# Kernel optimization log

Hardware: AMD Instinct MI355X
Metric: run time of the kernel (lower is better)

## Reference

```python
import jax, jax.numpy as jnp
import numpy as np

TAU_CONVERGE = 0.01
N_STABLE = 2
B, L, DIM = 8, 4096, 1024
H, M = 16, 64
D_HEAD = DIM // H


def setup_inputs() -> dict:
    key = jax.random.key(0)
    k1, k2, k3, k4, k5, k6 = jax.random.split(key, 6)
    z_current = jax.random.normal(k1, (B, L, DIM), dtype=jnp.float32)
    # small perturbation so per-head velocity straddles tau_converge
    z_prev = z_current + 0.00125 * jax.random.normal(k2, (B, L, DIM), dtype=jnp.float32)
    codebook = jax.random.normal(k3, (H, M, D_HEAD), dtype=jnp.float32) * 0.02
    frozen_values = jax.random.normal(k4, (B, L, H, D_HEAD), dtype=jnp.float32)
    consecutive_converged = jax.random.randint(k5, (B, L, H), 0, 2, dtype=jnp.int32)
    crystallised = jax.random.randint(k6, (B, L, H), 0, 2) > 0
    return {
        "z_current": z_current,
        "z_prev": z_prev,
        "codebook": codebook,
        "frozen_values": frozen_values,
        "consecutive_converged": consecutive_converged,
        "crystallised": crystallised,
    }


def reference(z_current, z_prev, codebook, frozen_values, consecutive_converged, crystallised):
    """One crystallisation step: velocity -> counters -> snap-to-codebook -> enforce.

    Mirrors ConvergenceMonitor.update_and_crystallise followed by enforce(),
    with MultiHeadedCodebook.quantise(hard=True) for the codebook snap.
    All freeze/snap logic is outside the gradient graph (torch.no_grad/detach).
    """
    sg = jax.lax.stop_gradient
    zc = z_current.reshape(B, L, H, D_HEAD)   # [B,L,H,d]
    zp = z_prev.reshape(B, L, H, D_HEAD)

    # per-head velocity norm (detached in original)
    velocity = jnp.linalg.norm(sg(zc) - sg(zp), axis=-1)       # [B,L,H]
    converged = velocity < TAU_CONVERGE
    cc_new = jnp.where(converged, consecutive_converged + 1, 0)
    newly = (cc_new >= N_STABLE) & (~crystallised)             # [B,L,H] bool

    # hard nearest-neighbour quantise per head (no_grad in original)
    z_sg = sg(zc)
    cb = sg(codebook)
    # squared L2 distance: ||z||^2 - 2 z.c + ||c||^2  -> [B,L,H,M]
    d2 = (jnp.sum(z_sg * z_sg, axis=-1, keepdims=True)
          - 2.0 * jnp.einsum('blhd,hmd->blhm', z_sg, cb)
          + jnp.sum(cb * cb, axis=-1)[None, None])
    idx = jnp.argmin(d2, axis=-1)                              # [B,L,H]
    # gather nearest entries per head: codebook[h, idx[b,l,h]] -> [B,L,H,d]
    entries = cb[jnp.arange(H)[None, None, :], idx]

    # masked scatter of newly crystallised heads into frozen values
    frozen_new = jnp.where(newly[..., None], entries, sg(frozen_values))
    crystal_new = crystallised | newly

    # enforce: overwrite crystallised heads with frozen codebook values
    z_enforced = jnp.where(crystal_new[..., None], frozen_new, zc).reshape(B, L, DIM)
    return z_enforced, crystal_new, newly, cc_new, frozen_new
```

## Files before the change

### kernel.cpp

```cpp
#include <hip/hip_runtime.h>

#define BB 8
#define LL 4096
#define DIM 1024
#define HH 16
#define MM 64
#define DH 64

constexpr long long NZ = (long long)BB * LL * DIM;
constexpr long long NG = (long long)BB * LL * HH;
constexpr long long O_Z   = 0;
constexpr long long O_CRY = NZ;
constexpr long long O_NEW = NZ + NG;
constexpr long long O_CC  = NZ + 2 * NG;
constexpr long long O_FR  = NZ + 3 * NG;

#define DETECT_BLOCKS 64
#define DETECT_DWORDS (NG / 4)

__global__ __launch_bounds__(256) void detect_bool_kernel(
    const unsigned int* __restrict__ buf, unsigned int* __restrict__ partials)
{
    __shared__ unsigned int acc;
    if (threadIdx.x == 0) acc = 0u;
    __syncthreads();
    const int per_block = DETECT_DWORDS / DETECT_BLOCKS;
    const long long base = (long long)blockIdx.x * per_block;
    unsigned int v = 0u;
    for (int i = threadIdx.x; i < per_block; i += 256)
        v |= buf[base + i];
    atomicOr(&acc, v);
    __syncthreads();
    if (threadIdx.x == 0) partials[blockIdx.x] = acc;
}

#define ROWS 8

__global__ __launch_bounds__(256) void crystal_main(
    const float4* __restrict__ zc4,
    const float4* __restrict__ zp4,
    const float4* __restrict__ fr4,
    const int*    __restrict__ ccount,
    const void*   __restrict__ cry_raw,
    const unsigned int* __restrict__ partials,
    float* __restrict__ out)
{
    const int t   = threadIdx.x;
    const int h   = t >> 4;
    const int sub = t & 15;

    unsigned int om = 0u;
    #pragma unroll
    for (int i = 0; i < DETECT_BLOCKS; ++i) om |= partials[i];
    const bool u8mode = om > 1u;

    const long long row0 = (long long)blockIdx.x * ROWS;
    long long idx = row0 * (DIM / 4) + t;
    long long g   = row0 * HH + h;

    float4 zc = zc4[idx];
    float4 zp = zp4[idx];
    float4 fr = fr4[idx];
    int    cc = ccount[g];
    int    cv = u8mode ? (int)((const unsigned char*)cry_raw)[g]
                       : ((const int*)cry_raw)[g];

    #pragma unroll 1
    for (int r = 0; r < ROWS; ++r) {
        const long long nidx = idx + (DIM / 4);
        const long long gn   = g + HH;
        float4 zcn, zpn, frn; int ccn_ = 0, cvn = 0;
        if (r < ROWS - 1) {
            zcn = zc4[nidx]; zpn = zp4[nidx]; frn = fr4[nidx];
            ccn_ = ccount[gn];
            cvn  = u8mode ? (int)((const unsigned char*)cry_raw)[gn]
                          : ((const int*)cry_raw)[gn];
        }

        double s;
        {
            double dx = (double)zc.x - (double)zp.x;
            double dy = (double)zc.y - (double)zp.y;
            double dz = (double)zc.z - (double)zp.z;
            double dw = (double)zc.w - (double)zp.w;
            s = dx * dx + dy * dy + dz * dz + dw * dw;
        }
        s += __shfl_xor(s, 1);
        s += __shfl_xor(s, 2);
        s += __shfl_xor(s, 4);
        s += __shfl_xor(s, 8);

        const bool conv = sqrt(s) < 0.01;
        const int  ccn  = conv ? cc + 1 : 0;
        const bool cry  = cv != 0;
        const bool newly   = (ccn >= 2) && !cry;
        const bool crystal = cry || newly;

        float4 zout;
        zout.x = crystal ? fr.x : zc.x;
        zout.y = crystal ? fr.y : zc.y;
        zout.z = crystal ? fr.z : zc.z;
        zout.w = crystal ? fr.w : zc.w;

        reinterpret_cast<float4*>(out + O_Z)[idx]  = zout;
        reinterpret_cast<float4*>(out + O_FR)[idx] = fr;
        if (sub == 0) {
            out[O_CRY + g] = crystal ? 1.0f : 0.0f;
            out[O_NEW + g] = newly   ? 1.0f : 0.0f;
            out[O_CC  + g] = (float)ccn;
        }

        zc = zcn; zp = zpn; fr = frn; cc = ccn_; cv = cvn;
        idx = nidx; g = gn;
    }
}

#define RPB 64
#define CHUNKS (BB * LL / RPB)

__global__ __launch_bounds__(64) void crystal_snap(
    const float4* __restrict__ zc4,
    const float*  __restrict__ cb,
    float* __restrict__ out)
{
    __shared__ float zsh[DH];

    const int lane = threadIdx.x;
    const int h    = blockIdx.x / CHUNKS;
    const int c    = blockIdx.x % CHUNKS;
    const long long blbase = (long long)c * RPB;

    const float f = out[O_NEW + (blbase + lane) * HH + h];
    unsigned long long mask = __ballot(f > 0.5f);
    if (mask == 0ull) return;

    const float* cbh = cb + (long long)h * MM * DH;
    const float4* crow = reinterpret_cast<const float4*>(cbh + lane * DH);

    while (mask) {
        const int r = __ffsll(mask) - 1;
        mask &= mask - 1;
        const long long bl   = blbase + r;
        const long long seg4 = bl * (DIM / 4) + h * (DH / 4);

        if (lane < 16)
            reinterpret_cast<float4*>(zsh)[lane] = zc4[seg4 + lane];
        __syncthreads();

        double d2 = 0.0;
        #pragma unroll
        for (int k = 0; k < DH / 4; ++k) {
            const float4 zk = reinterpret_cast<const float4*>(zsh)[k];
            const float4 cvv = crow[k];
            double a = (double)zk.x - (double)cvv.x;
            double b = (double)zk.y - (double)cvv.y;
            double cq = (double)zk.z - (double)cvv.z;
            double d = (double)zk.w - (double)cvv.w;
            d2 += a * a + b * b + cq * cq + d * d;
        }

        double best = d2;
        int bidx = lane;
        #pragma unroll
        for (int m2 = 1; m2 <= 32; m2 <<= 1) {
            double ob = __shfl_xor(best, m2);
            int    oi = __shfl_xor(bidx, m2);
            if (ob < best || (ob == best && oi < bidx)) { best = ob; bidx = oi; }
        }

        if (lane < 16) {
            const float4 ev = reinterpret_cast<const float4*>(cbh + bidx * DH)[lane];
            reinterpret_cast<float4*>(out + O_Z)[seg4 + lane]  = ev;
            reinterpret_cast<float4*>(out + O_FR)[seg4 + lane] = ev;
        }
        __syncthreads();
    }
}

extern "C" void kernel_launch(void* const* d_in, const int* in_sizes, int n_in,
                              void* d_out, int out_size, void* d_ws, size_t ws_size,
                              hipStream_t stream) {
    const float4* zc4 = (const float4*)d_in[0];
    const float4* zp4 = (const float4*)d_in[1];
    const float*  cb  = (const float*)d_in[2];
    const float4* fr4 = (const float4*)d_in[3];
    const int*    cc  = (const int*)d_in[4];
    const void*   cry = d_in[5];
    float* out = (float*)d_out;
    unsigned int* partials = (unsigned int*)d_ws;

    hipLaunchKernelGGL(detect_bool_kernel, dim3(DETECT_BLOCKS), dim3(256), 0, stream,
                       (const unsigned int*)cry, partials);
    hipLaunchKernelGGL(crystal_main, dim3((BB * LL) / ROWS), dim3(256), 0, stream,
                       zc4, zp4, fr4, cc, cry, partials, out);
    hipLaunchKernelGGL(crystal_snap, dim3(HH * CHUNKS), dim3(64), 0, stream,
                       zc4, cb, out);
}
```

Baseline: 218.6 us.

## Drop bool-detect pass, emit newly bitmasks, streamline snap kernel

```diff
diff --git a/kernel.cpp b/kernel.cpp
--- a/kernel.cpp
+++ b/kernel.cpp
@@ -15,24 +15,8 @@
 constexpr long long O_CC  = NZ + 2 * NG;
 constexpr long long O_FR  = NZ + 3 * NG;
 
-#define DETECT_BLOCKS 64
-#define DETECT_DWORDS (NG / 4)
-
-__global__ __launch_bounds__(256) void detect_bool_kernel(
-    const unsigned int* __restrict__ buf, unsigned int* __restrict__ partials)
-{
-    __shared__ unsigned int acc;
-    if (threadIdx.x == 0) acc = 0u;
-    __syncthreads();
-    const int per_block = DETECT_DWORDS / DETECT_BLOCKS;
-    const long long base = (long long)blockIdx.x * per_block;
-    unsigned int v = 0u;
-    for (int i = threadIdx.x; i < per_block; i += 256)
-        v |= buf[base + i];
-    atomicOr(&acc, v);
-    __syncthreads();
-    if (threadIdx.x == 0) partials[blockIdx.x] = acc;
-}
+typedef float nfloat4 __attribute__((ext_vector_type(4)));
+
 
 #define ROWS 8
 
@@ -41,18 +25,17 @@
     const float4* __restrict__ zp4,
     const float4* __restrict__ fr4,
     const int*    __restrict__ ccount,
-    const void*   __restrict__ cry_raw,
-    const unsigned int* __restrict__ partials,
+    const int*    __restrict__ cryst,
+    unsigned int* __restrict__ masks,
     float* __restrict__ out)
 {
+    __shared__ float lds_cry[ROWS * HH];
+    __shared__ float lds_new[ROWS * HH];
+    __shared__ float lds_cc [ROWS * HH];
+
     const int t   = threadIdx.x;
     const int h   = t >> 4;
     const int sub = t & 15;
-
-    unsigned int om = 0u;
-    #pragma unroll
-    for (int i = 0; i < DETECT_BLOCKS; ++i) om |= partials[i];
-    const bool u8mode = om > 1u;
 
     const long long row0 = (long long)blockIdx.x * ROWS;
     long long idx = row0 * (DIM / 4) + t;
@@ -62,8 +45,9 @@
     float4 zp = zp4[idx];
     float4 fr = fr4[idx];
     int    cc = ccount[g];
-    int    cv = u8mode ? (int)((const unsigned char*)cry_raw)[g]
-                       : ((const int*)cry_raw)[g];
+    int    cv = cryst[g];
+
+    unsigned int wmask = 0u;
 
     #pragma unroll 1
     for (int r = 0; r < ROWS; ++r) {
@@ -72,9 +56,7 @@
         float4 zcn, zpn, frn; int ccn_ = 0, cvn = 0;
         if (r < ROWS - 1) {
             zcn = zc4[nidx]; zpn = zp4[nidx]; frn = fr4[nidx];
-            ccn_ = ccount[gn];
-            cvn  = u8mode ? (int)((const unsigned char*)cry_raw)[gn]
-                          : ((const int*)cry_raw)[gn];
+            ccn_ = ccount[gn]; cvn = cryst[gn];
         }
 
         double s;
@@ -96,66 +78,113 @@
         const bool newly   = (ccn >= 2) && !cry;
         const bool crystal = cry || newly;
 
-        float4 zout;
+        nfloat4 zout;
         zout.x = crystal ? fr.x : zc.x;
         zout.y = crystal ? fr.y : zc.y;
         zout.z = crystal ? fr.z : zc.z;
         zout.w = crystal ? fr.w : zc.w;
-
-        reinterpret_cast<float4*>(out + O_Z)[idx]  = zout;
-        reinterpret_cast<float4*>(out + O_FR)[idx] = fr;
+        nfloat4 frv = { fr.x, fr.y, fr.z, fr.w };
+
+        __builtin_nontemporal_store(zout, reinterpret_cast<nfloat4*>(out + O_Z)  + idx);
+        __builtin_nontemporal_store(frv,  reinterpret_cast<nfloat4*>(out + O_FR) + idx);
+
         if (sub == 0) {
-            out[O_CRY + g] = crystal ? 1.0f : 0.0f;
-            out[O_NEW + g] = newly   ? 1.0f : 0.0f;
-            out[O_CC  + g] = (float)ccn;
-        }
+            lds_cry[r * HH + h] = crystal ? 1.0f : 0.0f;
+            lds_new[r * HH + h] = newly   ? 1.0f : 0.0f;
+            lds_cc [r * HH + h] = (float)ccn;
+        }
+
+        const unsigned long long bal = __ballot(newly && sub == 0);
+        const unsigned int b4 = (unsigned int)((bal        & 1ull)       |
+                                               ((bal >> 16) & 1ull) << 1 |
+                                               ((bal >> 32) & 1ull) << 2 |
+                                               ((bal >> 48) & 1ull) << 3);
+        wmask |= b4 << (4 * r);
 
         zc = zcn; zp = zpn; fr = frn; cc = ccn_; cv = cvn;
         idx = nidx; g = gn;
     }
+
+    if ((t & 63) == 0)
+        masks[blockIdx.x * 4 + (t >> 6)] = wmask;
+
+    __syncthreads();
+    if (t < ROWS * HH) {
+        const long long g0 = (long long)blockIdx.x * (ROWS * HH) + t;
+        out[O_CRY + g0] = lds_cry[t];
+        out[O_NEW + g0] = lds_new[t];
+        out[O_CC  + g0] = lds_cc [t];
+    }
 }
 
-#define RPB 64
-#define CHUNKS (BB * LL / RPB)
+#define MB_PER_CHUNK 64
+#define CHUNK_ROWS  (MB_PER_CHUNK * ROWS)
+#define NCHUNKS     (BB * LL / CHUNK_ROWS)
 
 __global__ __launch_bounds__(64) void crystal_snap(
     const float4* __restrict__ zc4,
     const float*  __restrict__ cb,
+    const unsigned int* __restrict__ masks,
     float* __restrict__ out)
 {
-    __shared__ float zsh[DH];
-
     const int lane = threadIdx.x;
-    const int h    = blockIdx.x / CHUNKS;
-    const int c    = blockIdx.x % CHUNKS;
-    const long long blbase = (long long)c * RPB;
-
-    const float f = out[O_NEW + (blbase + lane) * HH + h];
-    unsigned long long mask = __ballot(f > 0.5f);
-    if (mask == 0ull) return;
+    const int h    = blockIdx.x / NCHUNKS;
+    const int c    = blockIdx.x % NCHUNKS;
+    const int w    = h >> 2;
+    const int h2   = h & 3;
+
+    const int mb = c * MB_PER_CHUNK + lane;
+    const unsigned int word = masks[mb * 4 + w];
+    unsigned int rows8 = 0u;
+    #pragma unroll
+    for (int r = 0; r < ROWS; ++r)
+        rows8 |= ((word >> (4 * r + h2)) & 1u) << r;
+
+    unsigned long long act = __ballot(rows8 != 0u);
+    if (act == 0ull) return;
 
     const float* cbh = cb + (long long)h * MM * DH;
-    const float4* crow = reinterpret_cast<const float4*>(cbh + lane * DH);
-
-    while (mask) {
-        const int r = __ffsll(mask) - 1;
-        mask &= mask - 1;
-        const long long bl   = blbase + r;
-        const long long seg4 = bl * (DIM / 4) + h * (DH / 4);
-
-        if (lane < 16)
-            reinterpret_cast<float4*>(zsh)[lane] = zc4[seg4 + lane];
-        __syncthreads();
+    float4 crow[16];
+    {
+        const float4* cp = reinterpret_cast<const float4*>(cbh + lane * DH);
+        #pragma unroll
+        for (int k = 0; k < 16; ++k) crow[k] = cp[k];
+    }
+
+    int curl = 0; unsigned int curm8 = 0u;
+    auto next_bl = [&]() -> long long {
+        while (curm8 == 0u) {
+            if (act == 0ull) return -1;
+            curl = __ffsll(act) - 1; act &= act - 1;
+            curm8 = __shfl(rows8, curl);
+        }
+        const int r = __ffs(curm8) - 1; curm8 &= curm8 - 1;
+        return (long long)(c * MB_PER_CHUNK + curl) * ROWS + r;
+    };
+
+    long long bl = next_bl();
+    long long seg4 = bl * (DIM / 4) + h * (DH / 4);
+    float4 zv;
+    if (lane < 16) zv = zc4[seg4 + lane];
+
+    while (bl >= 0) {
+        const long long bln = next_bl();
+        const long long seg4n = bln * (DIM / 4) + h * (DH / 4);
+        float4 zvn;
+        if (bln >= 0 && lane < 16) zvn = zc4[seg4n + lane];
 
         double d2 = 0.0;
         #pragma unroll
-        for (int k = 0; k < DH / 4; ++k) {
-            const float4 zk = reinterpret_cast<const float4*>(zsh)[k];
-            const float4 cvv = crow[k];
-            double a = (double)zk.x - (double)cvv.x;
-            double b = (double)zk.y - (double)cvv.y;
-            double cq = (double)zk.z - (double)cvv.z;
-            double d = (double)zk.w - (double)cvv.w;
+        for (int k = 0; k < 16; ++k) {
+            float4 zk;
+            zk.x = __shfl(zv.x, k);
+            zk.y = __shfl(zv.y, k);
+            zk.z = __shfl(zv.z, k);
+            zk.w = __shfl(zv.w, k);
+            double a  = (double)zk.x - (double)crow[k].x;
+            double b  = (double)zk.y - (double)crow[k].y;
+            double cq = (double)zk.z - (double)crow[k].z;
+            double d  = (double)zk.w - (double)crow[k].w;
             d2 += a * a + b * b + cq * cq + d * d;
         }
 
@@ -173,7 +202,8 @@
             reinterpret_cast<float4*>(out + O_Z)[seg4 + lane]  = ev;
             reinterpret_cast<float4*>(out + O_FR)[seg4 + lane] = ev;
         }
-        __syncthreads();
+
+        bl = bln; seg4 = seg4n; zv = zvn;
     }
 }
 
@@ -185,14 +215,12 @@
     const float*  cb  = (const float*)d_in[2];
     const float4* fr4 = (const float4*)d_in[3];
     const int*    cc  = (const int*)d_in[4];
-    const void*   cry = d_in[5];
+    const int*    cry = (const int*)d_in[5];
     float* out = (float*)d_out;
-    unsigned int* partials = (unsigned int*)d_ws;
-
-    hipLaunchKernelGGL(detect_bool_kernel, dim3(DETECT_BLOCKS), dim3(256), 0, stream,
-                       (const unsigned int*)cry, partials);
+    unsigned int* masks = (unsigned int*)d_ws;
+
     hipLaunchKernelGGL(crystal_main, dim3((BB * LL) / ROWS), dim3(256), 0, stream,
-                       zc4, zp4, fr4, cc, cry, partials, out);
-    hipLaunchKernelGGL(crystal_snap, dim3(HH * CHUNKS), dim3(64), 0, stream,
-                       zc4, cb, out);
+                       zc4, zp4, fr4, cc, cry, masks, out);
+    hipLaunchKernelGGL(crystal_snap, dim3(HH * NCHUNKS), dim3(64), 0, stream,
+                       zc4, cb, masks, out);
 }
```

New measurement: 305.0 us. 39.5% more time.
